# Kernel tuning notes

Measured on AMD Instinct MI355X. Metric: run time of the kernel, lower is better.

## Reference

```python
import jax, jax.numpy as jnp
import numpy as np

ALPHA = 0.2  # LeakyReLU negative slope
N, IN_DIM, OUT_DIM = 8192, 512, 64


def setup_inputs() -> dict:
    key = jax.random.key(0)
    k1, k2, k3, k4 = jax.random.split(key, 4)
    X = jax.random.normal(k1, (N, IN_DIM), dtype=jnp.float32)
    Adj = jax.random.randint(k2, (N, N), 0, 2, dtype=jnp.int32)
    # xavier_uniform with gain=1.414
    def xavier(k, shape, gain=1.414):
        fan_in, fan_out = shape[0], shape[1]
        bound = gain * np.sqrt(6.0 / (fan_in + fan_out))
        return jax.random.uniform(k, shape, jnp.float32, -bound, bound)
    W = xavier(k3, (IN_DIM, OUT_DIM))
    a = xavier(k4, (2 * OUT_DIM, 1))
    return {"X": X, "Adj": Adj, "W": W, "a": a}


def reference(X, Adj, W, a):
    # h = X @ W : [N, D]
    h = X @ W
    D = h.shape[1]
    # Decompose pairwise score: concat([h_i, h_j]) @ a == h_i @ a1 + h_j @ a2
    s1 = h @ a[:D, 0]   # [N] -- contribution of row (destination) node i
    s2 = h @ a[D:, 0]   # [N] -- contribution of column (source) node j
    e = jnp.exp(jax.nn.leaky_relu(s1[:, None] + s2[None, :], negative_slope=ALPHA))  # [N, N]
    e = jnp.where(Adj == 0, jnp.float32(0.0), e)
    attention = e / jnp.sum(e, axis=1, keepdims=True)
    # dropout is a no-op in eval mode (training=False)
    return attention @ h
```

## Files before the change

kernel.cpp:

```cpp
#include <hip/hip_runtime.h>
#include <math.h>


#define NN 8192
#define KIN 512
#define DD 64
#define ALPHA 0.2f

__global__ __launch_bounds__(256) void k_gemm_h(const float* __restrict__ X,
                                                const float* __restrict__ W,
                                                float* __restrict__ h) {
    __shared__ __align__(16) float XT[32 * 68];
    __shared__ __align__(16) float WL[32 * 64];
    const int t = threadIdx.x;
    const int i0 = blockIdx.x * 64;
    const int rb = t >> 4, db = t & 15;
    float acc[4][4] = {};

    for (int k0 = 0; k0 < KIN; k0 += 32) {
        {
            const int kq = t & 7;
            const int rr = t >> 3;
#pragma unroll
            for (int p = 0; p < 2; ++p) {
                const int row = p * 32 + rr;
                const float4 x4 = *(const float4*)(X + (size_t)(i0 + row) * KIN + k0 + kq * 4);
                XT[(kq * 4 + 0) * 68 + row] = x4.x;
                XT[(kq * 4 + 1) * 68 + row] = x4.y;
                XT[(kq * 4 + 2) * 68 + row] = x4.z;
                XT[(kq * 4 + 3) * 68 + row] = x4.w;
            }
#pragma unroll
            for (int p = 0; p < 2; ++p) {
                const int q = p * 256 + t;
                const int kk = q >> 4, dq = q & 15;
                *(float4*)(WL + kk * 64 + dq * 4) =
                    *(const float4*)(W + (size_t)(k0 + kk) * DD + dq * 4);
            }
        }
        __syncthreads();
#pragma unroll
        for (int k = 0; k < 32; ++k) {
            const float4 a4 = *(const float4*)(XT + k * 68 + rb * 4);
            const float4 b4 = *(const float4*)(WL + k * 64 + db * 4);
            const float av[4] = {a4.x, a4.y, a4.z, a4.w};
            const float bv[4] = {b4.x, b4.y, b4.z, b4.w};
#pragma unroll
            for (int i = 0; i < 4; ++i)
#pragma unroll
                for (int j = 0; j < 4; ++j) acc[i][j] += av[i] * bv[j];
        }
        __syncthreads();
    }
#pragma unroll
    for (int i = 0; i < 4; ++i) {
        float4 o = {acc[i][0], acc[i][1], acc[i][2], acc[i][3]};
        *(float4*)(h + (size_t)(i0 + rb * 4 + i) * DD + db * 4) = o;
    }
}

__global__ __launch_bounds__(256) void k_s12(const float* __restrict__ h,
                                             const float* __restrict__ a,
                                             float* __restrict__ s1,
                                             float* __restrict__ s2) {
    const int lane = threadIdx.x & 63;
    const int w = threadIdx.x >> 6;
    const int r = blockIdx.x * 4 + w;
    const float v = h[(size_t)r * DD + lane];
    float p1 = v * a[lane];
    float p2 = v * a[64 + lane];
#pragma unroll
    for (int off = 32; off; off >>= 1) {
        p1 += __shfl_xor(p1, off, 64);
        p2 += __shfl_xor(p2, off, 64);
    }
    if (lane == 0) {
        s1[r] = p1;
        s2[r] = p2;
    }
}

__global__ __launch_bounds__(256) void k_attn(const float* __restrict__ h,
                                              const int* __restrict__ Adj,
                                              const float* __restrict__ s1,
                                              const float* __restrict__ s2,
                                              float* __restrict__ numP,
                                              float* __restrict__ denP) {
    __shared__ __align__(16) float ET[64 * 65];
    __shared__ __align__(16) float HL[64 * 64];
    const int t = threadIdx.x;
    const int it = blockIdx.x >> 3;
    const int jc = blockIdx.x & 7;
    const int i0 = it * 64;
    const int jb0 = jc * 1024;
    const int jl = t & 63, rg = t >> 6;
    const int rb = t >> 4, db = t & 15;

    float s1v[16];
#pragma unroll
    for (int rr = 0; rr < 16; ++rr) s1v[rr] = s1[i0 + rg * 16 + rr];
    float dd[16] = {};
    float nn[4][4] = {};

    for (int w = 0; w < 16; ++w) {
        const int jb = jb0 + w * 64;
#pragma unroll
        for (int p = 0; p < 4; ++p) {
            const int q = p * 256 + t;
            *(float4*)(HL + q * 4) = *(const float4*)(h + (size_t)jb * DD + q * 4);
        }
        const float s2l = s2[jb + jl];
        const int* adjp = Adj + (size_t)(i0 + rg * 16) * NN + jb + jl;
#pragma unroll
        for (int rr = 0; rr < 16; ++rr) {
            const int adj = adjp[(size_t)rr * NN];
            const float s = s1v[rr] + s2l;
            const float l = s > 0.f ? s : ALPHA * s;
            float e = __expf(l);
            e = (adj != 0) ? e : 0.f;
            ET[jl * 65 + rg * 16 + rr] = e;
            dd[rr] += e;
        }
        __syncthreads();
#pragma unroll 8
        for (int jj = 0; jj < 64; ++jj) {
            const float4 hv = *(const float4*)(HL + jj * 64 + db * 4);
            const float e0 = ET[jj * 65 + rb * 4 + 0];
            const float e1 = ET[jj * 65 + rb * 4 + 1];
            const float e2 = ET[jj * 65 + rb * 4 + 2];
            const float e3 = ET[jj * 65 + rb * 4 + 3];
            nn[0][0] += e0 * hv.x; nn[0][1] += e0 * hv.y; nn[0][2] += e0 * hv.z; nn[0][3] += e0 * hv.w;
            nn[1][0] += e1 * hv.x; nn[1][1] += e1 * hv.y; nn[1][2] += e1 * hv.z; nn[1][3] += e1 * hv.w;
            nn[2][0] += e2 * hv.x; nn[2][1] += e2 * hv.y; nn[2][2] += e2 * hv.z; nn[2][3] += e2 * hv.w;
            nn[3][0] += e3 * hv.x; nn[3][1] += e3 * hv.y; nn[3][2] += e3 * hv.z; nn[3][3] += e3 * hv.w;
        }
        __syncthreads();
    }
    const size_t base = (size_t)blockIdx.x * 64 * 64;
#pragma unroll
    for (int i = 0; i < 4; ++i) {
        float4 o = {nn[i][0], nn[i][1], nn[i][2], nn[i][3]};
        *(float4*)(numP + base + (size_t)(rb * 4 + i) * 64 + db * 4) = o;
    }
#pragma unroll
    for (int rr = 0; rr < 16; ++rr) {
        float v = dd[rr];
#pragma unroll
        for (int off = 32; off; off >>= 1) v += __shfl_xor(v, off, 64);
        if (jl == 0) denP[(size_t)blockIdx.x * 64 + rg * 16 + rr] = v;
    }
}

__global__ __launch_bounds__(256) void k_final(const float* __restrict__ numP,
                                               const float* __restrict__ denP,
                                               float* __restrict__ out) {
    const int idx = blockIdx.x * 256 + threadIdx.x;
    const int i = idx >> 6, d = idx & 63;
    const int it = i >> 6, r = i & 63;
    float num = 0.f, den = 0.f;
#pragma unroll
    for (int c = 0; c < 8; ++c) {
        const size_t bx = (size_t)(it * 8 + c);
        num += numP[bx * 4096 + (size_t)r * 64 + d];
        den += denP[bx * 64 + r];
    }
    out[idx] = num / den;
}

extern "C" void kernel_launch(void* const* d_in, const int* in_sizes, int n_in,
                              void* d_out, int out_size, void* d_ws, size_t ws_size,
                              hipStream_t stream) {
    const float* X = (const float*)d_in[0];
    const int* Adj = (const int*)d_in[1];
    const float* W = (const float*)d_in[2];
    const float* a = (const float*)d_in[3];
    float* out = (float*)d_out;

    float* ws = (float*)d_ws;
    float* h = ws;
    float* s1 = h + 524288;
    float* s2 = s1 + 8192;
    float* numP = s2 + 8192;
    float* denP = numP + 1024 * 4096;

    k_gemm_h<<<128, 256, 0, stream>>>(X, W, h);
    k_s12<<<2048, 256, 0, stream>>>(h, a, s1, s2);
    k_attn<<<1024, 256, 0, stream>>>(h, Adj, s1, s2, numP, denP);
    k_final<<<2048, 256, 0, stream>>>(numP, denP, out);
}
```

Baseline: 453.7 us.

## Use bf16 MFMA for attention aggregation with pre-swizzled h fragments

Replaces the scalar FP32 LDS-tiled attention kernel with an MFMA 16x16x32 bf16 kernel. Each wave computes exp scores straight into A-fragments while reading Adj rows as vectorized int4 loads. A new kernel pre-packs h into bf16 B-fragment layout so the main loop needs no LDS or syncs. The h GEMM also gets smaller 32-row tiles to launch more blocks. The cost is bf16 precision on the attention weights and h, which may affect accuracy, plus one extra small kernel launch.

```diff
diff --git a/kernel.cpp b/kernel.cpp
--- a/kernel.cpp
+++ b/kernel.cpp
@@ -7,29 +7,28 @@
 #define DD 64
 #define ALPHA 0.2f
 
+using floatx4 = __attribute__((ext_vector_type(4))) float;
+using bf16x8  = __attribute__((ext_vector_type(8))) __bf16;
+
 __global__ __launch_bounds__(256) void k_gemm_h(const float* __restrict__ X,
                                                 const float* __restrict__ W,
                                                 float* __restrict__ h) {
-    __shared__ __align__(16) float XT[32 * 68];
+    __shared__ __align__(16) float XT[32 * 36];
     __shared__ __align__(16) float WL[32 * 64];
     const int t = threadIdx.x;
-    const int i0 = blockIdx.x * 64;
-    const int rb = t >> 4, db = t & 15;
-    float acc[4][4] = {};
+    const int i0 = blockIdx.x * 32;
+    const int rb = t >> 5;
+    const int db = t & 31;
+    float acc[4][2] = {};
 
     for (int k0 = 0; k0 < KIN; k0 += 32) {
         {
-            const int kq = t & 7;
-            const int rr = t >> 3;
-#pragma unroll
-            for (int p = 0; p < 2; ++p) {
-                const int row = p * 32 + rr;
-                const float4 x4 = *(const float4*)(X + (size_t)(i0 + row) * KIN + k0 + kq * 4);
-                XT[(kq * 4 + 0) * 68 + row] = x4.x;
-                XT[(kq * 4 + 1) * 68 + row] = x4.y;
-                XT[(kq * 4 + 2) * 68 + row] = x4.z;
-                XT[(kq * 4 + 3) * 68 + row] = x4.w;
-            }
+            const int row = t >> 3, kq = t & 7;
+            const float4 x4 = *(const float4*)(X + (size_t)(i0 + row) * KIN + k0 + kq * 4);
+            XT[(kq * 4 + 0) * 36 + row] = x4.x;
+            XT[(kq * 4 + 1) * 36 + row] = x4.y;
+            XT[(kq * 4 + 2) * 36 + row] = x4.z;
+            XT[(kq * 4 + 3) * 36 + row] = x4.w;
 #pragma unroll
             for (int p = 0; p < 2; ++p) {
                 const int q = p * 256 + t;
@@ -41,21 +40,21 @@
         __syncthreads();
 #pragma unroll
         for (int k = 0; k < 32; ++k) {
-            const float4 a4 = *(const float4*)(XT + k * 68 + rb * 4);
-            const float4 b4 = *(const float4*)(WL + k * 64 + db * 4);
-            const float av[4] = {a4.x, a4.y, a4.z, a4.w};
-            const float bv[4] = {b4.x, b4.y, b4.z, b4.w};
+            const float4 xa = *(const float4*)(XT + k * 36 + rb * 4);
+            const float2 wb = *(const float2*)(WL + k * 64 + db * 2);
+            const float xv[4] = {xa.x, xa.y, xa.z, xa.w};
 #pragma unroll
-            for (int i = 0; i < 4; ++i)
-#pragma unroll
-                for (int j = 0; j < 4; ++j) acc[i][j] += av[i] * bv[j];
+            for (int i = 0; i < 4; ++i) {
+                acc[i][0] += xv[i] * wb.x;
+                acc[i][1] += xv[i] * wb.y;
+            }
         }
         __syncthreads();
     }
 #pragma unroll
     for (int i = 0; i < 4; ++i) {
-        float4 o = {acc[i][0], acc[i][1], acc[i][2], acc[i][3]};
-        *(float4*)(h + (size_t)(i0 + rb * 4 + i) * DD + db * 4) = o;
+        float2 o = {acc[i][0], acc[i][1]};
+        *(float2*)(h + (size_t)(i0 + rb * 4 + i) * DD + db * 2) = o;
     }
 }
 
@@ -80,75 +79,76 @@
     }
 }
 
-__global__ __launch_bounds__(256) void k_attn(const float* __restrict__ h,
-                                              const int* __restrict__ Adj,
-                                              const float* __restrict__ s1,
-                                              const float* __restrict__ s2,
-                                              float* __restrict__ numP,
-                                              float* __restrict__ denP) {
-    __shared__ __align__(16) float ET[64 * 65];
-    __shared__ __align__(16) float HL[64 * 64];
+__global__ __launch_bounds__(256) void k_hfrag(const float* __restrict__ h,
+                                               __bf16* __restrict__ hFrag) {
+    const int f = blockIdx.x * 256 + threadIdx.x;
+    const int lane = f & 63, dt = (f >> 6) & 3, jblk = f >> 8;
+    const int n = lane & 15, q = lane >> 4;
+    bf16x8 v;
+#pragma unroll
+    for (int jj = 0; jj < 8; ++jj)
+        v[jj] = (__bf16)h[(size_t)(jblk * 32 + q * 8 + jj) * DD + dt * 16 + n];
+    *(bf16x8*)(hFrag + (size_t)f * 8) = v;
+}
+
+__global__ __launch_bounds__(256) void k_attn2(const bf16x8* __restrict__ hFrag,
+                                               const int* __restrict__ Adj,
+                                               const float* __restrict__ s1,
+                                               const float* __restrict__ s2,
+                                               float* __restrict__ numP,
+                                               float* __restrict__ denP) {
     const int t = threadIdx.x;
-    const int it = blockIdx.x >> 3;
-    const int jc = blockIdx.x & 7;
+    const int wv = t >> 6;
+    const int lane = t & 63;
+    const int n = lane & 15, q = lane >> 4;
+    const int it = blockIdx.x >> 3, jc = blockIdx.x & 7;
     const int i0 = it * 64;
-    const int jb0 = jc * 1024;
-    const int jl = t & 63, rg = t >> 6;
-    const int rb = t >> 4, db = t & 15;
+    const int row = i0 + wv * 16 + n;
+    const float s1v = s1[row];
+    const int jbase = jc * 1024;
 
-    float s1v[16];
+    floatx4 acc[4] = {};
+    float den = 0.f;
+
+    const int* adjRow = Adj + (size_t)row * NN;
+
+    for (int ks = 0; ks < 32; ++ks) {
+        const int j0 = jbase + ks * 32;
+        const int jq = j0 + q * 8;
+        const int4 a0 = *(const int4*)(adjRow + jq);
+        const int4 a1 = *(const int4*)(adjRow + jq + 4);
+        const float4 z0 = *(const float4*)(s2 + jq);
+        const float4 z1 = *(const float4*)(s2 + jq + 4);
+        const int adjv[8] = {a0.x, a0.y, a0.z, a0.w, a1.x, a1.y, a1.z, a1.w};
+        const float s2v[8] = {z0.x, z0.y, z0.z, z0.w, z1.x, z1.y, z1.z, z1.w};
+        bf16x8 af;
 #pragma unroll
-    for (int rr = 0; rr < 16; ++rr) s1v[rr] = s1[i0 + rg * 16 + rr];
-    float dd[16] = {};
-    float nn[4][4] = {};
+        for (int u = 0; u < 8; ++u) {
+            const float s = s1v + s2v[u];
+            const float l = fmaxf(s, ALPHA * s);
+            float e = __expf(l);
+            e = adjv[u] ? e : 0.f;
+            den += e;
+            af[u] = (__bf16)e;
+        }
+        const bf16x8* hf = hFrag + ((size_t)(j0 >> 5) * 4) * 64 + lane;
+#pragma unroll
+        for (int dt = 0; dt < 4; ++dt) {
+            const bf16x8 bf = hf[dt * 64];
+            acc[dt] = __builtin_amdgcn_mfma_f32_16x16x32_bf16(af, bf, acc[dt], 0, 0, 0);
+        }
+    }
 
-    for (int w = 0; w < 16; ++w) {
-        const int jb = jb0 + w * 64;
+    const size_t base = (size_t)blockIdx.x * 4096;
 #pragma unroll
-        for (int p = 0; p < 4; ++p) {
-            const int q = p * 256 + t;
-            *(float4*)(HL + q * 4) = *(const float4*)(h + (size_t)jb * DD + q * 4);
-        }
-        const float s2l = s2[jb + jl];
-        const int* adjp = Adj + (size_t)(i0 + rg * 16) * NN + jb + jl;
+    for (int dt = 0; dt < 4; ++dt)
 #pragma unroll
-        for (int rr = 0; rr < 16; ++rr) {
-            const int adj = adjp[(size_t)rr * NN];
-            const float s = s1v[rr] + s2l;
-            const float l = s > 0.f ? s : ALPHA * s;
-            float e = __expf(l);
-            e = (adj != 0) ? e : 0.f;
-            ET[jl * 65 + rg * 16 + rr] = e;
-            dd[rr] += e;
-        }
-        __syncthreads();
-#pragma unroll 8
-        for (int jj = 0; jj < 64; ++jj) {
-            const float4 hv = *(const float4*)(HL + jj * 64 + db * 4);
-            const float e0 = ET[jj * 65 + rb * 4 + 0];
-            const float e1 = ET[jj * 65 + rb * 4 + 1];
-            const float e2 = ET[jj * 65 + rb * 4 + 2];
-            const float e3 = ET[jj * 65 + rb * 4 + 3];
-            nn[0][0] += e0 * hv.x; nn[0][1] += e0 * hv.y; nn[0][2] += e0 * hv.z; nn[0][3] += e0 * hv.w;
-            nn[1][0] += e1 * hv.x; nn[1][1] += e1 * hv.y; nn[1][2] += e1 * hv.z; nn[1][3] += e1 * hv.w;
-            nn[2][0] += e2 * hv.x; nn[2][1] += e2 * hv.y; nn[2][2] += e2 * hv.z; nn[2][3] += e2 * hv.w;
-            nn[3][0] += e3 * hv.x; nn[3][1] += e3 * hv.y; nn[3][2] += e3 * hv.z; nn[3][3] += e3 * hv.w;
-        }
-        __syncthreads();
-    }
-    const size_t base = (size_t)blockIdx.x * 64 * 64;
-#pragma unroll
-    for (int i = 0; i < 4; ++i) {
-        float4 o = {nn[i][0], nn[i][1], nn[i][2], nn[i][3]};
-        *(float4*)(numP + base + (size_t)(rb * 4 + i) * 64 + db * 4) = o;
-    }
-#pragma unroll
-    for (int rr = 0; rr < 16; ++rr) {
-        float v = dd[rr];
-#pragma unroll
-        for (int off = 32; off; off >>= 1) v += __shfl_xor(v, off, 64);
-        if (jl == 0) denP[(size_t)blockIdx.x * 64 + rg * 16 + rr] = v;
-    }
+        for (int r = 0; r < 4; ++r)
+            numP[base + (size_t)(wv * 16 + q * 4 + r) * 64 + dt * 16 + n] = acc[dt][r];
+
+    den += __shfl_xor(den, 16, 64);
+    den += __shfl_xor(den, 32, 64);
+    if (q == 0) denP[(size_t)blockIdx.x * 64 + wv * 16 + n] = den;
 }
 
 __global__ __launch_bounds__(256) void k_final(const float* __restrict__ numP,
@@ -180,11 +180,13 @@
     float* h = ws;
     float* s1 = h + 524288;
     float* s2 = s1 + 8192;
-    float* numP = s2 + 8192;
+    __bf16* hFrag = (__bf16*)(s2 + 8192);
+    float* numP = s2 + 8192 + 262144;
     float* denP = numP + 1024 * 4096;
 
-    k_gemm_h<<<128, 256, 0, stream>>>(X, W, h);
+    k_gemm_h<<<256, 256, 0, stream>>>(X, W, h);
     k_s12<<<2048, 256, 0, stream>>>(h, a, s1, s2);
-    k_attn<<<1024, 256, 0, stream>>>(h, Adj, s1, s2, numP, denP);
+    k_hfrag<<<256, 256, 0, stream>>>(h, hFrag);
+    k_attn2<<<1024, 256, 0, stream>>>((const bf16x8*)hFrag, Adj, s1, s2, numP, denP);
     k_final<<<2048, 256, 0, stream>>>(numP, denP, out);
 }
```

New measurement: 432.3 us. 1.05x faster.
